# Kernel optimization log

Measured on AMD Instinct MI355X. Metric: run time of the kernel, lower is better.

## Reference

```python
import jax, jax.numpy as jnp
import numpy as np

K_MASK = -2.3819763e+38
B, T, D = 2, 2048, 2048
N, K, H = 8, 2, 256          # query heads, kv heads, head dim
F = 8192                     # ffn hidden
A = 4                        # num_altup_inputs
P = 4                        # num_modalities
WINDOW = 512
SOFT_CAP = 50.0
Q_SCALE = H ** -0.5
ROPE_BASE = 10000.0


def rms_norm(x, scale=None, eps=1e-6):
    y = x * jax.lax.rsqrt(jnp.mean(jnp.square(x), axis=-1, keepdims=True) + eps)
    if scale is not None:
        y = y * (1.0 + scale)   # scale_plus_one=True
    return y


def apply_rope(x, pos, base=ROPE_BASE, scale_factor=1.0):
    # x: [B,T,num_heads,H], pos: [B,T]
    h = x.shape[-1]
    frac = 2.0 * jnp.arange(h // 2, dtype=jnp.float32) / h
    timescale = base ** frac
    sin_inp = (pos[..., None].astype(jnp.float32) / timescale)[..., None, :] / scale_factor  # [B,T,1,H/2]
    sin, cos = jnp.sin(sin_inp), jnp.cos(sin_inp)
    x1, x2 = jnp.split(x, 2, axis=-1)
    return jnp.concatenate([x1 * cos - x2 * sin, x2 * cos + x1 * sin], axis=-1).astype(x.dtype)


def setup_inputs():
    key = jax.random.key(0)
    ks = jax.random.split(key, 12)
    r = lambda i, shape, s=0.02: jax.random.normal(ks[i], shape, dtype=jnp.float32) * s
    pos = jnp.broadcast_to(jnp.arange(T, dtype=jnp.int32), (B, T))
    causal = pos[:, :, None] >= pos[:, None, :]  # [B,T,T] bool
    return dict(
        x=jax.random.normal(ks[0], (A, B, T, D), dtype=jnp.float32),
        segment_pos=pos,
        attn_mask=causal,
        router_w=r(1, (D, P), 1.0),
        pred_coefs=r(2, (P, A, A), 0.0001),
        corr_coefs=r(3, (P, A), 0.01),
        correct_output_scale=jnp.ones((D,), jnp.float32),
        pre_attn_scale=jnp.zeros((D,), jnp.float32),
        q_w=r(4, (N, D, H)),
        kv_w=r(5, (2, K, D, H)),
        qk_q_scale=jnp.zeros((H,), jnp.float32),
        qk_k_scale=jnp.zeros((H,), jnp.float32),
        o_w=r(6, (N, H, D)),
        post_attn_scale=jnp.zeros((D,), jnp.float32),
        pre_ffw_scale=jnp.zeros((D,), jnp.float32),
        gate_w=r(7, (D, F)),
        up_w=r(8, (D, F)),
        down_w=r(9, (F, D)),
        post_ffw_scale=jnp.zeros((D,), jnp.float32),
    )


def _router(h, router_w):
    # modality router: scale by 1/d_model, project, tanh in fp32
    return jnp.tanh(jnp.einsum('btd,dp->btp', h * (1.0 / D), router_w).astype(jnp.float32))


def _attention(x, segment_pos, attn_mask, q_w, kv_w, qk_q_scale, qk_k_scale, o_w):
    q = jnp.einsum('btd,ndh->btnh', x, q_w)               # [B,T,N,H]
    k, v = jnp.einsum('bsd,ckdh->cbskh', x, kv_w)         # each [B,T,K,H]
    q = rms_norm(q, qk_q_scale)                           # qk norm
    k = rms_norm(k, qk_k_scale)
    v = rms_norm(v)                                       # value norm (no scale)
    q = apply_rope(q, segment_pos) * Q_SCALE
    k = apply_rope(k, segment_pos)
    g = N // K                                            # GQA group size
    qr = q.reshape(B, T, K, g, H)
    logits = jnp.einsum('btkgh,bskh->btkgs', qr, k).reshape(B, T, N, T)
    logits = jnp.tanh(logits / SOFT_CAP) * SOFT_CAP       # attn_logits_soft_cap
    # sliding-window mask combined with causal attn_mask
    sliding = (segment_pos[:, None, :] > segment_pos[:, :, None] - WINDOW) & \
              (segment_pos[:, None, :] < segment_pos[:, :, None] + WINDOW)
    mask = attn_mask & sliding
    padded = jnp.where(mask[:, :, None, :], logits, K_MASK)
    probs = jax.nn.softmax(padded, axis=-1).astype(k.dtype)
    enc = jnp.einsum('btkgs,bskh->btkgh', probs.reshape(B, T, K, g, T), v).reshape(B, T, N, H)
    return jnp.einsum('btnh,nhd->btd', enc, o_w)


def reference(x, segment_pos, attn_mask, router_w, pred_coefs, corr_coefs,
              correct_output_scale, pre_attn_scale, q_w, kv_w, qk_q_scale, qk_k_scale,
              o_w, post_attn_scale, pre_ffw_scale, gate_w, up_w, down_w, post_ffw_scale):
    # ---- AltUp predict ----
    mods = _router(x[0], router_w)                                   # [B,T,P]
    coefs = jnp.einsum('btp,pij->btij', mods, pred_coefs.astype(jnp.float32))
    predictions = x + jnp.einsum('btij,jbtd->ibtd', coefs, x).astype(x.dtype)
    active = predictions[0]
    # ---- attention block ----
    attn_in = rms_norm(active, pre_attn_scale)
    attn = _attention(attn_in, segment_pos, attn_mask, q_w, kv_w, qk_q_scale, qk_k_scale, o_w)
    attn = rms_norm(attn, post_attn_scale)
    attn_gated = active + attn
    # ---- gated-GELU MLP ----
    h = rms_norm(attn_gated, pre_ffw_scale)
    ffw = jnp.einsum('btf,fd->btd', jax.nn.gelu(h @ gate_w) * (h @ up_w), down_w)
    ffw = rms_norm(ffw, post_ffw_scale)
    activated = attn_gated + ffw
    # ---- AltUp correct (with scale_corrected_output) ----
    activated = activated * correct_output_scale
    mods_c = _router(activated, router_w)
    c = jnp.einsum('btp,pi->bti', mods_c, corr_coefs.astype(jnp.float32)) + 1.0
    innovation = activated - predictions[0]
    corrected = predictions + jnp.einsum('bti,btd->ibtd', c, innovation).astype(x.dtype)
    return corrected
```

## Files before the change

### kernel.cpp

```cpp
#include <hip/hip_runtime.h>
#include <hip/hip_bf16.h>

typedef unsigned short u16;
typedef __attribute__((ext_vector_type(8))) short bf16x8_t;
typedef __attribute__((ext_vector_type(4))) float f32x4_t;

#define DEV __device__ __forceinline__

constexpr int cB = 2, cT = 2048, cD = 2048;
constexpr int cN = 8, cK = 2, cH = 256, cF = 8192;
constexpr int cBT = cB * cT;
constexpr float cEPS = 1e-6f;
constexpr float cQS = 0.0625f;
constexpr float cCAP = 50.0f;
constexpr int cWIN = 512;
constexpr int cNH = 12;

DEV u16 f2bf(float f) {
  union { float f; unsigned u; } c; c.f = f;
  unsigned u = c.u;
  return (u16)((u + 0x7fffu + ((u >> 16) & 1u)) >> 16);
}
DEV float bf2f(u16 h) {
  union { unsigned u; float f; } c; c.u = ((unsigned)h) << 16;
  return c.f;
}
DEV float g4(const float4& v, int k) { return k == 0 ? v.x : k == 1 ? v.y : k == 2 ? v.z : v.w; }
DEV void store_bf4(u16* p, float a, float b, float c, float d) {
  union { u16 h[4]; uint2 v; } o;
  o.h[0] = f2bf(a); o.h[1] = f2bf(b); o.h[2] = f2bf(c); o.h[3] = f2bf(d);
  *(uint2*)p = o.v;
}
DEV float tanh_fast(float x) {
  float e2 = __expf(2.0f * x);
  return 1.0f - 2.0f * __builtin_amdgcn_rcpf(e2 + 1.0f);
}
DEV float gelu_fast(float x) {
  float u = 1.5957691216057308f * (x + 0.044715f * x * x * x);
  float e2 = __expf(u);
  return x * (1.0f - __builtin_amdgcn_rcpf(e2 + 1.0f));
}

DEV float block_sum256(float v, float* sbuf) {
  #pragma unroll
  for (int m = 32; m > 0; m >>= 1) v += __shfl_xor(v, m, 64);
  int wid = threadIdx.x >> 6;
  if ((threadIdx.x & 63) == 0) sbuf[wid] = v;
  __syncthreads();
  float tot = sbuf[0] + sbuf[1] + sbuf[2] + sbuf[3];
  __syncthreads();
  return tot;
}
DEV void block_sum256x4(float v[4], float* sbuf ) {
  #pragma unroll
  for (int m = 32; m > 0; m >>= 1) {
    #pragma unroll
    for (int k = 0; k < 4; k++) v[k] += __shfl_xor(v[k], m, 64);
  }
  int wid = threadIdx.x >> 6;
  if ((threadIdx.x & 63) == 0) *(float4*)(sbuf + wid * 4) = make_float4(v[0], v[1], v[2], v[3]);
  __syncthreads();
  #pragma unroll
  for (int k = 0; k < 4; k++) v[k] = sbuf[k] + sbuf[4 + k] + sbuf[8 + k] + sbuf[12 + k];
  __syncthreads();
}

#define GLD_LDS16(gp, lp) __builtin_amdgcn_global_load_lds( \
    (const __attribute__((address_space(1))) void*)(gp),    \
    (__attribute__((address_space(3))) void*)(lp), 16, 0, 0)

#define WAITV(n) asm volatile("s_waitcnt vmcnt(" #n ")" ::: "memory")
#define SCHED0() __builtin_amdgcn_sched_barrier(0)

__global__ __launch_bounds__(256) void k_transpose_cast(
    const float* __restrict__ src, u16* __restrict__ dst, int R, int C, int gu) {
  __shared__ float tile[64][65];
  size_t base = (size_t)blockIdx.z * R * C;
  int c0 = blockIdx.x * 64, r0 = blockIdx.y * 64;
  int tx = threadIdx.x & 15, ty = threadIdx.x >> 4;
  #pragma unroll
  for (int i = 0; i < 4; i++) {
    int r = ty + i * 16;
    float4 v = *(const float4*)(src + base + (size_t)(r0 + r) * C + c0 + tx * 4);
    tile[r][tx * 4 + 0] = v.x; tile[r][tx * 4 + 1] = v.y;
    tile[r][tx * 4 + 2] = v.z; tile[r][tx * 4 + 3] = v.w;
  }
  __syncthreads();
  #pragma unroll
  for (int i = 0; i < 4; i++) {
    int j = ty + i * 16;
    int c = c0 + j;
    int n = (gu < 0) ? c : (((c >> 4) << 5) + (gu << 4) + (c & 15));
    store_bf4(dst + base + (size_t)n * R + r0 + tx * 4,
              tile[tx * 4 + 0][j], tile[tx * 4 + 1][j],
              tile[tx * 4 + 2][j], tile[tx * 4 + 3][j]);
  }
}

__global__ __launch_bounds__(256) void k_rope_table(
    const int* __restrict__ pos, float2* __restrict__ rt) {
  int idx = blockIdx.x * 256 + threadIdx.x;
  int bt = idx >> 7, j = idx & 127;
  float p = (float)pos[bt];
  float ts = powf(10000.0f, (2.0f * j) * (1.0f / cH));
  float si = p / ts;
  rt[idx] = make_float2(sinf(si), cosf(si));
}

__global__ __launch_bounds__(256) void k_predict(
    const float* __restrict__ x, const float* __restrict__ router_w,
    const float* __restrict__ pred_coefs, const float* __restrict__ pre_attn_scale,
    float* __restrict__ out, u16* __restrict__ attn_in) {
  __shared__ float sbuf[16];
  int bt = blockIdx.x, tid = threadIdx.x;
  const size_t PL = (size_t)cBT * cD;
  const size_t rowb = (size_t)bt * cD;
  float4 xv[4][2];
  #pragma unroll
  for (int j = 0; j < 4; j++)
    #pragma unroll
    for (int u = 0; u < 2; u++)
      xv[j][u] = *(const float4*)(x + j * PL + rowb + (u * 256 + tid) * 4);
  float rp[4] = {0, 0, 0, 0};
  #pragma unroll
  for (int u = 0; u < 2; u++)
    #pragma unroll
    for (int k = 0; k < 4; k++) {
      int e = (u * 256 + tid) * 4 + k;
      float4 rw = *(const float4*)(router_w + (size_t)e * 4);
      float xe = g4(xv[0][u], k);
      rp[0] += xe * rw.x; rp[1] += xe * rw.y; rp[2] += xe * rw.z; rp[3] += xe * rw.w;
    }
  block_sum256x4(rp, sbuf);
  float mods[4];
  #pragma unroll
  for (int p = 0; p < 4; p++) mods[p] = tanh_fast(rp[p] * (1.0f / cD));
  float coef[4][4];
  #pragma unroll
  for (int i = 0; i < 4; i++)
    #pragma unroll
    for (int j = 0; j < 4; j++) {
      float s = 0;
      #pragma unroll
      for (int p = 0; p < 4; p++) s += mods[p] * pred_coefs[(p * 4 + i) * 4 + j];
      coef[i][j] = s;
    }
  float4 p04[2]; float ssq = 0;
  #pragma unroll
  for (int u = 0; u < 2; u++)
    #pragma unroll
    for (int i = 0; i < 4; i++) {
      float4 s = xv[i][u];
      #pragma unroll
      for (int j = 0; j < 4; j++) {
        s.x += coef[i][j] * xv[j][u].x; s.y += coef[i][j] * xv[j][u].y;
        s.z += coef[i][j] * xv[j][u].z; s.w += coef[i][j] * xv[j][u].w;
      }
      *(float4*)(out + i * PL + rowb + (u * 256 + tid) * 4) = s;
      if (i == 0) { p04[u] = s; ssq += s.x * s.x + s.y * s.y + s.z * s.z + s.w * s.w; }
    }
  float rs = rsqrtf(block_sum256(ssq, sbuf) * (1.0f / cD) + cEPS);
  #pragma unroll
  for (int u = 0; u < 2; u++) {
    int e0 = (u * 256 + tid) * 4;
    float4 sc = *(const float4*)(pre_attn_scale + e0);
    store_bf4(attn_in + rowb + e0,
              p04[u].x * rs * (1.0f + sc.x), p04[u].y * rs * (1.0f + sc.y),
              p04[u].z * rs * (1.0f + sc.z), p04[u].w * rs * (1.0f + sc.w));
  }
}

template <int OUT_MODE>
__global__ __launch_bounds__(512, 2) void k_gemm8w(
    const u16* __restrict__ A, const u16* __restrict__ Bt, void* __restrict__ Cv,
    int Nn, int Kk) {
  constexpr int MI = 8;
  constexpr int A_KS = 256 * 32;
  constexpr int B_KS = 256 * 32;
  constexpr int BUF_E = 2 * A_KS + 2 * B_KS;
  extern __shared__ u16 lds[];

  const int tid = threadIdx.x;
  const int wid = tid >> 6, lane = tid & 63;
  const int wr = wid >> 2, wc = wid & 3;
  const int fr = lane & 15, fq = lane >> 4;

  const int nwg = gridDim.x * gridDim.y;
  const int flat = blockIdx.y * gridDim.x + blockIdx.x;
  const int swz = (flat & 7) * (nwg >> 3) + (flat >> 3);
  const int m0 = (swz % gridDim.x) * 256;
  const int n0 = (swz / gridDim.x) * 256;
  const int NT = Kk >> 6;

  const int srow = lane >> 2, sslot = lane & 3;
  const int scol = (sslot ^ ((srow >> 1) & 3)) * 8;
  const u16* aSrc0 = A + (size_t)(m0 + wid * 16 + srow) * Kk + scol;
  const u16* aSrc1 = A + (size_t)(m0 + 128 + wid * 16 + srow) * Kk + scol;
  const u16* bSrc0 = Bt + (size_t)(n0 + wid * 16 + srow) * Kk + scol;
  const u16* bSrc1 = Bt + (size_t)(n0 + 128 + wid * 16 + srow) * Kk + scol;
  const int swzR = (fq ^ ((fr >> 1) & 3)) * 8;
  const int aoff = (wr * 128 + fr) * 32 + swzR;
  const int boff = 2 * A_KS + (wc * 64 + fr) * 32 + swzR;

  auto stageA = [&](int t, int ks) {
    u16* dst = lds + (t & 1) * BUF_E + ks * A_KS + wid * 16 * 32;
    int koff = t * 64 + ks * 32;
    GLD_LDS16(aSrc0 + koff, dst);
    GLD_LDS16(aSrc1 + koff, dst + 128 * 32);
  };
  auto stageB = [&](int t, int ks) {
    u16* dst = lds + (t & 1) * BUF_E + 2 * A_KS + ks * B_KS + wid * 16 * 32;
    int koff = t * 64 + ks * 32;
    GLD_LDS16(bSrc0 + koff, dst);
    GLD_LDS16(bSrc1 + koff, dst + 128 * 32);
  };

  f32x4_t acc[MI][4];
  #pragma unroll
  for (int i = 0; i < MI; i++)
    #pragma unroll
    for (int j = 0; j < 4; j++) acc[i][j] = (f32x4_t){0.f, 0.f, 0.f, 0.f};

  bf16x8_t a0[MI], bP[2], bQ[2];

#define RD_A(bufp, ks, i) (*(const bf16x8_t*)((bufp) + aoff + (ks) * A_KS + (i) * 512))
#define RD_B(bufp, ks, j) (*(const bf16x8_t*)((bufp) + boff + (ks) * B_KS + (j) * 512))

#define MFMA_CLUSTER(av, bv, J0)                                                     \
  __builtin_amdgcn_s_setprio(1);                                                     \
  _Pragma("unroll")                                                                  \
  for (int i = 0; i < MI; i++) {                                                     \
    acc[i][J0]     = __builtin_amdgcn_mfma_f32_16x16x32_bf16(av[i], bv[0], acc[i][J0], 0, 0, 0);     \
    acc[i][J0 + 1] = __builtin_amdgcn_mfma_f32_16x16x32_bf16(av[i], bv[1], acc[i][J0 + 1], 0, 0, 0); \
  }                                                                                  \
  __builtin_amdgcn_s_setprio(0);

  stageA(0, 0); stageB(0, 0); stageA(0, 1); stageB(0, 1);
  stageA(1, 0); stageB(1, 0);
  WAITV(8);
  __builtin_amdgcn_s_barrier();
  SCHED0();
  bP[0] = RD_B(lds, 0, 0); bP[1] = RD_B(lds, 0, 1);

  for (int t = 0; t < NT; t++) {
    const u16* buf = lds + (t & 1) * BUF_E;
    const u16* bufn = lds + ((t + 1) & 1) * BUF_E;
    const bool p1 = (t + 1 < NT), p2 = (t + 2 < NT);

    #pragma unroll
    for (int i = 0; i < MI; i++) a0[i] = RD_A(buf, 0, i);
    if (p1) stageA(t + 1, 1);
    __builtin_amdgcn_s_barrier();
    SCHED0();
    bQ[0] = RD_B(buf, 0, 2); bQ[1] = RD_B(buf, 0, 3);
    MFMA_CLUSTER(a0, bP, 0)
    __builtin_amdgcn_s_barrier();

    if (p1) stageB(t + 1, 1);
    if (p1) WAITV(8); else WAITV(0);
    __builtin_amdgcn_s_barrier();
    SCHED0();
    bP[0] = RD_B(buf, 1, 0); bP[1] = RD_B(buf, 1, 1);
    MFMA_CLUSTER(a0, bQ, 2)
    __builtin_amdgcn_s_barrier();

    #pragma unroll
    for (int i = 0; i < MI; i++) a0[i] = RD_A(buf, 1, i);
    if (p2) stageA(t + 2, 0);
    __builtin_amdgcn_s_barrier();
    SCHED0();
    bQ[0] = RD_B(buf, 1, 2); bQ[1] = RD_B(buf, 1, 3);
    MFMA_CLUSTER(a0, bP, 0)
    __builtin_amdgcn_s_barrier();

    if (p2) stageB(t + 2, 0);
    if (p2) WAITV(8); else if (p1) WAITV(4);
    __builtin_amdgcn_s_barrier();
    SCHED0();
    if (p1) { bP[0] = RD_B(bufn, 0, 0); bP[1] = RD_B(bufn, 0, 1); }
    MFMA_CLUSTER(a0, bQ, 2)
    __builtin_amdgcn_s_barrier();
  }
#undef MFMA_CLUSTER
#undef RD_A
#undef RD_B

  if constexpr (OUT_MODE == 2) {
    const int Nh = Nn >> 1;
    #pragma unroll
    for (int i = 0; i < MI; i++)
      #pragma unroll
      for (int jp = 0; jp < 2; jp++) {
        int c = (n0 + wc * 64 + jp * 32) / 2 + fr;
        #pragma unroll
        for (int r = 0; r < 4; r++) {
          int m = m0 + wr * (MI * 16) + i * 16 + fq * 4 + r;
          float g = acc[i][2 * jp][r], uu = acc[i][2 * jp + 1][r];
          ((u16*)Cv)[(size_t)m * Nh + c] = f2bf(gelu_fast(g) * uu);
        }
      }
  } else {
    #pragma unroll
    for (int i = 0; i < MI; i++)
      #pragma unroll
      for (int j = 0; j < 4; j++)
        #pragma unroll
        for (int r = 0; r < 4; r++) {
          int m = m0 + wr * (MI * 16) + i * 16 + fq * 4 + r;
          int n = n0 + wc * 64 + j * 16 + fr;
          ((u16*)Cv)[(size_t)m * Nn + n] = f2bf(acc[i][j][r]);
        }
  }
}

template <int OUT_MODE>
__global__ __launch_bounds__(512, 2) void k_gemm4r(
    const u16* __restrict__ A, const u16* __restrict__ Bt, void* __restrict__ Cv,
    int Nn, int Kk) {
  constexpr int MI = 4;
  constexpr int BM = 128;
  constexpr int A_KS = BM * 32;
  constexpr int B_KS = 256 * 32;
  constexpr int SLOT_E = 2 * A_KS + 2 * B_KS;
  extern __shared__ u16 lds[];

  const int tid = threadIdx.x;
  const int wid = tid >> 6, lane = tid & 63;
  const int wr = wid >> 2, wc = wid & 3;
  const int fr = lane & 15, fq = lane >> 4;

  const int nwg = gridDim.x * gridDim.y;
  const int flat = blockIdx.y * gridDim.x + blockIdx.x;
  const int swz = (flat & 7) * (nwg >> 3) + (flat >> 3);
  const int m0 = (swz % gridDim.x) * BM;
  const int n0 = (swz / gridDim.x) * 256;
  const int NT = Kk >> 6;

  const int srow = lane >> 2, sslot = lane & 3;

  auto stageA = [&](int t, int ks) {
    u16* buf = lds + (t % 3) * SLOT_E + ks * A_KS;
    int row0 = wid * 16;
    int row = row0 + srow;
    int col = (sslot ^ ((row >> 1) & 3)) * 8;
    GLD_LDS16(A + (size_t)(m0 + row) * Kk + t * 64 + ks * 32 + col, buf + row0 * 32);
  };
  auto stageB = [&](int t, int ks) {
    u16* buf = lds + (t % 3) * SLOT_E + 2 * A_KS + ks * B_KS;
    #pragma unroll
    for (int i = 0; i < 2; i++) {
      int row0 = i * 128 + wid * 16;
      int row = row0 + srow;
      int col = (sslot ^ ((row >> 1) & 3)) * 8;
      GLD_LDS16(Bt + (size_t)(n0 + row) * Kk + t * 64 + ks * 32 + col, buf + row0 * 32);
    }
  };
  auto readA = [&](const u16* buf, int ks, int i) -> bf16x8_t {
    int row = wr * 64 + i * 16 + fr;
    return *(const bf16x8_t*)(buf + ks * A_KS + row * 32 + (fq ^ ((row >> 1) & 3)) * 8);
  };
  auto readB = [&](const u16* buf, int ks, int j) -> bf16x8_t {
    int row = wc * 64 + j * 16 + fr;
    return *(const bf16x8_t*)(buf + 2 * A_KS + ks * B_KS + row * 32 + (fq ^ ((row >> 1) & 3)) * 8);
  };

  f32x4_t acc[MI][4];
  #pragma unroll
  for (int i = 0; i < MI; i++)
    #pragma unroll
    for (int j = 0; j < 4; j++) acc[i][j] = (f32x4_t){0.f, 0.f, 0.f, 0.f};

  stageA(0, 0); stageB(0, 0); stageA(0, 1); stageB(0, 1);
  stageA(1, 0); stageB(1, 0); stageA(1, 1); stageB(1, 1);
  WAITV(9);
  __builtin_amdgcn_s_barrier();

#define PHASE_MFMA4(J0)                                                             \
  __builtin_amdgcn_s_setprio(1);                                                    \
  _Pragma("unroll")                                                                 \
  for (int i = 0; i < MI; i++) {                                                    \
    acc[i][J0]     = __builtin_amdgcn_mfma_f32_16x16x32_bf16(a0[i], b0[0], acc[i][J0], 0, 0, 0);     \
    acc[i][J0 + 1] = __builtin_amdgcn_mfma_f32_16x16x32_bf16(a0[i], b0[1], acc[i][J0 + 1], 0, 0, 0); \
  }                                                                                 \
  __builtin_amdgcn_s_setprio(0);

  for (int t = 0; t < NT; t++) {
    const u16* buf = lds + (t % 3) * SLOT_E;
    const bool pf2 = (t + 2 < NT);
    const bool pf1 = (t + 1 < NT);
    bf16x8_t a0[MI], b0[2];

    #pragma unroll
    for (int i = 0; i < MI; i++) a0[i] = readA(buf, 0, i);
    b0[0] = readB(buf, 0, 0); b0[1] = readB(buf, 0, 1);
    if (pf2) stageA(t + 2, 0);
    __builtin_amdgcn_s_barrier();
    PHASE_MFMA4(0)
    __builtin_amdgcn_s_barrier();

    b0[0] = readB(buf, 0, 2); b0[1] = readB(buf, 0, 3);
    if (pf2) stageB(t + 2, 0);
    if (pf2) WAITV(9); else if (pf1) WAITV(6); else WAITV(0);
    __builtin_amdgcn_s_barrier();
    PHASE_MFMA4(2)
    __builtin_amdgcn_s_barrier();

    #pragma unroll
    for (int i = 0; i < MI; i++) a0[i] = readA(buf, 1, i);
    b0[0] = readB(buf, 1, 0); b0[1] = readB(buf, 1, 1);
    if (pf2) stageA(t + 2, 1);
    __builtin_amdgcn_s_barrier();
    PHASE_MFMA4(0)
    __builtin_amdgcn_s_barrier();

    b0[0] = readB(buf, 1, 2); b0[1] = readB(buf, 1, 3);
    if (pf2) stageB(t + 2, 1);
    if (pf2) WAITV(9); else if (pf1) WAITV(3);
    __builtin_amdgcn_s_barrier();
    PHASE_MFMA4(2)
    __builtin_amdgcn_s_barrier();
  }
#undef PHASE_MFMA4

  #pragma unroll
  for (int i = 0; i < MI; i++)
    #pragma unroll
    for (int j = 0; j < 4; j++)
      #pragma unroll
      for (int r = 0; r < 4; r++) {
        int m = m0 + wr * 64 + i * 16 + fq * 4 + r;
        int n = n0 + wc * 64 + j * 16 + fr;
        float v = acc[i][j][r];
        if (OUT_MODE == 1) ((u16*)Cv)[(size_t)m * Nn + n] = f2bf(v);
        else ((float*)Cv)[(size_t)m * Nn + n] = v;
      }
}

__global__ __launch_bounds__(64) void k_qkvpost(
    u16* __restrict__ qkv, const float* __restrict__ qscale,
    const float* __restrict__ kscale, const float2* __restrict__ rt,
    u16* __restrict__ vT) {
  int h = blockIdx.x % cNH, bt = blockIdx.x / cNH;
  int lane = threadIdx.x;
  u16* row = qkv + ((size_t)bt * cNH + h) * cH;
  float v[4], ssq = 0;
  #pragma unroll
  for (int m = 0; m < 4; m++) { v[m] = bf2f(row[lane + 64 * m]); ssq += v[m] * v[m]; }
  #pragma unroll
  for (int mm = 32; mm > 0; mm >>= 1) ssq += __shfl_xor(ssq, mm, 64);
  float rs = rsqrtf(ssq * (1.0f / cH) + cEPS);
  if (h < 10) {
    const float* sc = (h < 8) ? qscale : kscale;
    float os = (h < 8) ? cQS : 1.0f;
    #pragma unroll
    for (int m = 0; m < 4; m++) {
      int e = lane + 64 * m;
      v[m] = v[m] * rs * (1.0f + sc[e]);
    }
    #pragma unroll
    for (int m = 0; m < 2; m++) {
      int j = lane + 64 * m;
      float2 t = rt[bt * 128 + j];
      float x1 = v[m], x2 = v[m + 2];
      row[j]       = f2bf((x1 * t.y - x2 * t.x) * os);
      row[j + 128] = f2bf((x2 * t.y + x1 * t.x) * os);
    }
  } else {
    int kk = h - 10;
    int b = bt / cT, t = bt % cT;
    #pragma unroll
    for (int m = 0; m < 4; m++) {
      int e = lane + 64 * m;
      vT[((size_t)(b * cK + kk) * cH + e) * cT + t] = f2bf(v[m] * rs);
    }
  }
}

__global__ __launch_bounds__(64) void k_attn(
    const u16* __restrict__ qkv, const u16* __restrict__ vT, u16* __restrict__ enc) {
  int t0 = blockIdx.x * 16;
  int n = blockIdx.y, b = blockIdx.z;
  int kn = n >> 2;
  int lane = threadIdx.x;
  int fr = lane & 15, fq = lane >> 4;
  __shared__ float P[16][33];

  bf16x8_t qf[8];
  const u16* qrow = qkv + ((size_t)(b * cT + t0 + fr) * cNH + n) * cH;
  #pragma unroll
  for (int ks = 0; ks < 8; ks++) qf[ks] = *(const bf16x8_t*)(qrow + ks * 32 + fq * 8);

  f32x4_t acc[16];
  #pragma unroll
  for (int ht = 0; ht < 16; ht++) acc[ht] = (f32x4_t){0.f, 0.f, 0.f, 0.f};
  float psum[4] = {0.f, 0.f, 0.f, 0.f};

  int s_lo = t0 - (cWIN - 1); if (s_lo < 0) s_lo = 0; s_lo &= ~31;
  for (int s0 = s_lo; s0 <= t0 + 15; s0 += 32) {
    f32x4_t S[2];
    S[0] = (f32x4_t){0.f, 0.f, 0.f, 0.f};
    S[1] = (f32x4_t){0.f, 0.f, 0.f, 0.f};
    #pragma unroll
    for (int c = 0; c < 2; c++) {
      const u16* krow = qkv + ((size_t)(b * cT + s0 + c * 16 + fr) * cNH + 8 + kn) * cH;
      #pragma unroll
      for (int ks = 0; ks < 8; ks++) {
        bf16x8_t kf = *(const bf16x8_t*)(krow + ks * 32 + fq * 8);
        S[c] = __builtin_amdgcn_mfma_f32_16x16x32_bf16(qf[ks], kf, S[c], 0, 0, 0);
      }
    }
    #pragma unroll
    for (int c = 0; c < 2; c++) {
      int s = s0 + c * 16 + fr;
      #pragma unroll
      for (int r = 0; r < 4; r++) {
        int t = t0 + fq * 4 + r;
        float l = cCAP * tanh_fast(S[c][r] * (1.0f / cCAP));
        float pe = (s <= t && s >= t - (cWIN - 1)) ? __expf(l) : 0.0f;
        psum[r] += pe;
        P[fq * 4 + r][c * 16 + fr] = pe;
      }
    }
    bf16x8_t pf;
    #pragma unroll
    for (int e = 0; e < 8; e++) pf[e] = (short)f2bf(P[fr][fq * 8 + e]);
    #pragma unroll
    for (int ht = 0; ht < 16; ht++) {
      bf16x8_t vf = *(const bf16x8_t*)(vT + (((size_t)(b * cK + kn)) * cH + ht * 16 + fr) * cT + s0 + fq * 8);
      acc[ht] = __builtin_amdgcn_mfma_f32_16x16x32_bf16(pf, vf, acc[ht], 0, 0, 0);
    }
  }
  #pragma unroll
  for (int r = 0; r < 4; r++) {
    #pragma unroll
    for (int m = 1; m < 16; m <<= 1) psum[r] += __shfl_xor(psum[r], m, 64);
  }
  float inv[4];
  #pragma unroll
  for (int r = 0; r < 4; r++) inv[r] = 1.0f / psum[r];
  #pragma unroll
  for (int ht = 0; ht < 16; ht++)
    #pragma unroll
    for (int r = 0; r < 4; r++)
      enc[(((size_t)(b * cT + t0 + fq * 4 + r)) * cN + n) * cH + ht * 16 + fr] =
          f2bf(acc[ht][r] * inv[r]);
}

__global__ __launch_bounds__(256) void k_postattn(
    const float* __restrict__ attn_raw, const float* __restrict__ out0,
    const float* __restrict__ post_attn_scale, const float* __restrict__ pre_ffw_scale,
    float* __restrict__ ag, u16* __restrict__ h) {
  __shared__ float sbuf[4];
  int bt = blockIdx.x, tid = threadIdx.x;
  const size_t rowb = (size_t)bt * cD;
  float4 ar[2]; float ssq = 0;
  #pragma unroll
  for (int u = 0; u < 2; u++) {
    ar[u] = *(const float4*)(attn_raw + rowb + (u * 256 + tid) * 4);
    ssq += ar[u].x * ar[u].x + ar[u].y * ar[u].y + ar[u].z * ar[u].z + ar[u].w * ar[u].w;
  }
  float rs = rsqrtf(block_sum256(ssq, sbuf) * (1.0f / cD) + cEPS);
  float4 agv[2]; float ssq2 = 0;
  #pragma unroll
  for (int u = 0; u < 2; u++) {
    int e0 = (u * 256 + tid) * 4;
    float4 o0 = *(const float4*)(out0 + rowb + e0);
    float4 sc = *(const float4*)(post_attn_scale + e0);
    float4 a;
    a.x = o0.x + ar[u].x * rs * (1.0f + sc.x);
    a.y = o0.y + ar[u].y * rs * (1.0f + sc.y);
    a.z = o0.z + ar[u].z * rs * (1.0f + sc.z);
    a.w = o0.w + ar[u].w * rs * (1.0f + sc.w);
    agv[u] = a;
    *(float4*)(ag + rowb + e0) = a;
    ssq2 += a.x * a.x + a.y * a.y + a.z * a.z + a.w * a.w;
  }
  float rs2 = rsqrtf(block_sum256(ssq2, sbuf) * (1.0f / cD) + cEPS);
  #pragma unroll
  for (int u = 0; u < 2; u++) {
    int e0 = (u * 256 + tid) * 4;
    float4 sc = *(const float4*)(pre_ffw_scale + e0);
    store_bf4(h + rowb + e0,
              agv[u].x * rs2 * (1.0f + sc.x), agv[u].y * rs2 * (1.0f + sc.y),
              agv[u].z * rs2 * (1.0f + sc.z), agv[u].w * rs2 * (1.0f + sc.w));
  }
}

__global__ __launch_bounds__(256) void k_final(
    const float* __restrict__ ffw_raw, const float* __restrict__ ag,
    const float* __restrict__ post_ffw_scale, const float* __restrict__ cos_scale,
    const float* __restrict__ router_w, const float* __restrict__ corr_coefs,
    float* __restrict__ out) {
  __shared__ float sbuf[16];
  int bt = blockIdx.x, tid = threadIdx.x;
  const size_t PL = (size_t)cBT * cD;
  const size_t rowb = (size_t)bt * cD;
  float4 fv[2]; float ssq = 0;
  #pragma unroll
  for (int u = 0; u < 2; u++) {
    fv[u] = *(const float4*)(ffw_raw + rowb + (u * 256 + tid) * 4);
    ssq += fv[u].x * fv[u].x + fv[u].y * fv[u].y + fv[u].z * fv[u].z + fv[u].w * fv[u].w;
  }
  float rs = rsqrtf(block_sum256(ssq, sbuf) * (1.0f / cD) + cEPS);
  float4 av[2];
  float rp[4] = {0, 0, 0, 0};
  #pragma unroll
  for (int u = 0; u < 2; u++) {
    int e0 = (u * 256 + tid) * 4;
    float4 agx = *(const float4*)(ag + rowb + e0);
    float4 ps = *(const float4*)(post_ffw_scale + e0);
    float4 cs = *(const float4*)(cos_scale + e0);
    float4 a;
    a.x = (agx.x + fv[u].x * rs * (1.0f + ps.x)) * cs.x;
    a.y = (agx.y + fv[u].y * rs * (1.0f + ps.y)) * cs.y;
    a.z = (agx.z + fv[u].z * rs * (1.0f + ps.z)) * cs.z;
    a.w = (agx.w + fv[u].w * rs * (1.0f + ps.w)) * cs.w;
    av[u] = a;
    #pragma unroll
    for (int k = 0; k < 4; k++) {
      float4 rw = *(const float4*)(router_w + (size_t)(e0 + k) * 4);
      float xe = g4(a, k);
      rp[0] += xe * rw.x; rp[1] += xe * rw.y; rp[2] += xe * rw.z; rp[3] += xe * rw.w;
    }
  }
  block_sum256x4(rp, sbuf);
  float cc[4];
  #pragma unroll
  for (int i = 0; i < 4; i++) {
    float s = 1.0f;
    #pragma unroll
    for (int p = 0; p < 4; p++) s += tanh_fast(rp[p] * (1.0f / cD)) * corr_coefs[p * 4 + i];
    cc[i] = s;
  }
  #pragma unroll
  for (int u = 0; u < 2; u++) {
    size_t o = rowb + (u * 256 + tid) * 4;
    float4 p0 = *(const float4*)(out + o);
    float4 in4;
    in4.x = av[u].x - p0.x; in4.y = av[u].y - p0.y;
    in4.z = av[u].z - p0.z; in4.w = av[u].w - p0.w;
    float4 w0;
    w0.x = p0.x + cc[0] * in4.x; w0.y = p0.y + cc[0] * in4.y;
    w0.z = p0.z + cc[0] * in4.z; w0.w = p0.w + cc[0] * in4.w;
    *(float4*)(out + o) = w0;
    #pragma unroll
    for (int i = 1; i < 4; i++) {
      float4 q = *(const float4*)(out + i * PL + o);
      q.x += cc[i] * in4.x; q.y += cc[i] * in4.y;
      q.z += cc[i] * in4.z; q.w += cc[i] * in4.w;
      *(float4*)(out + i * PL + o) = q;
    }
  }
}

extern "C" void kernel_launch(void* const* d_in, const int* in_sizes, int n_in,
                              void* d_out, int out_size, void* d_ws, size_t ws_size,
                              hipStream_t stream) {
  const float* x              = (const float*)d_in[0];
  const int*   pos            = (const int*)d_in[1];
  const float* router_w       = (const float*)d_in[3];
  const float* pred_coefs     = (const float*)d_in[4];
  const float* corr_coefs     = (const float*)d_in[5];
  const float* cos_scale      = (const float*)d_in[6];
  const float* pre_attn_scale = (const float*)d_in[7];
  const float* q_w            = (const float*)d_in[8];
  const float* kv_w           = (const float*)d_in[9];
  const float* qk_q_scale     = (const float*)d_in[10];
  const float* qk_k_scale     = (const float*)d_in[11];
  const float* o_w            = (const float*)d_in[12];
  const float* post_attn_scale= (const float*)d_in[13];
  const float* pre_ffw_scale  = (const float*)d_in[14];
  const float* gate_w         = (const float*)d_in[15];
  const float* up_w           = (const float*)d_in[16];
  const float* down_w         = (const float*)d_in[17];
  const float* post_ffw_scale = (const float*)d_in[18];
  float* out = (float*)d_out;

  char* wsp = (char*)d_ws;
  size_t off = 0;
  auto take = [&](size_t nbytes) -> char* {
    char* p = wsp + off;
    off += (nbytes + 255) & ~((size_t)255);
    return p;
  };
  u16* gu_wT    = (u16*)take((size_t)2 * cF * cD * 2);
  u16* down_wT  = (u16*)take((size_t)cD * cF * 2);
  u16* qkv_wT   = (u16*)take((size_t)cNH * cH * cD * 2);
  u16* o_wT     = (u16*)take((size_t)cD * cN * cH * 2);
  u16* attn_in  = (u16*)take((size_t)cBT * cD * 2);
  u16* qkvbuf   = (u16*)take((size_t)cBT * cNH * cH * 2);
  u16* vTbuf    = (u16*)take((size_t)cB * cK * cH * cT * 2);
  u16* encbuf   = (u16*)take((size_t)cBT * cN * cH * 2);
  float* attn_raw = (float*)take((size_t)cBT * cD * 4);
  float* agbuf    = (float*)take((size_t)cBT * cD * 4);
  u16* hbuf     = (u16*)take((size_t)cBT * cD * 2);
  u16* Gcbuf    = (u16*)take((size_t)cBT * cF * 2);
  float* ffw_raw = (float*)take((size_t)cBT * cD * 4);
  float2* ropetab = (float2*)take((size_t)cBT * 128 * 8);
  (void)in_sizes; (void)n_in; (void)out_size; (void)ws_size;

  dim3 blk256(256), blk64(64), blk512(512);
  constexpr unsigned LDS8  = 2 * (2 * 256 * 32 + 2 * 256 * 32) * 2;
  constexpr unsigned LDS4R = 3 * (2 * 128 * 32 + 2 * 256 * 32) * 2;

  k_transpose_cast<<<dim3(cF / 64, cD / 64, 1), blk256, 0, stream>>>(gate_w, gu_wT, cD, cF, 0);
  k_transpose_cast<<<dim3(cF / 64, cD / 64, 1), blk256, 0, stream>>>(up_w, gu_wT, cD, cF, 1);
  k_transpose_cast<<<dim3(cD / 64, cF / 64, 1), blk256, 0, stream>>>(down_w, down_wT, cF, cD, -1);
  k_transpose_cast<<<dim3(cH / 64, cD / 64, cN), blk256, 0, stream>>>(q_w, qkv_wT, cD, cH, -1);
  k_transpose_cast<<<dim3(cH / 64, cD / 64, 2 * cK), blk256, 0, stream>>>(
      kv_w, qkv_wT + (size_t)cN * cH * cD, cD, cH, -1);
  k_transpose_cast<<<dim3(cD / 64, (cN * cH) / 64, 1), blk256, 0, stream>>>(o_w, o_wT, cN * cH, cD, -1);
  k_rope_table<<<dim3(cBT * 128 / 256), blk256, 0, stream>>>(pos, ropetab);

  k_predict<<<dim3(cBT), blk256, 0, stream>>>(x, router_w, pred_coefs, pre_attn_scale, out, attn_in);

  k_gemm4r<1><<<dim3(cBT / 128, (cNH * cH) / 256), blk512, LDS4R, stream>>>(
      attn_in, qkv_wT, qkvbuf, cNH * cH, cD);

  k_qkvpost<<<dim3(cBT * cNH), blk64, 0, stream>>>(qkvbuf, qk_q_scale, qk_k_scale, ropetab, vTbuf);

  k_attn<<<dim3(cT / 16, cN, cB), blk64, 0, stream>>>(qkvbuf, vTbuf, encbuf);

  k_gemm4r<0><<<dim3(cBT / 128, cD / 256), blk512, LDS4R, stream>>>(
      encbuf, o_wT, attn_raw, cD, cN * cH);
  k_postattn<<<dim3(cBT), blk256, 0, stream>>>(attn_raw, out, post_attn_scale, pre_ffw_scale, agbuf, hbuf);

  k_gemm8w<2><<<dim3(cBT / 256, (2 * cF) / 256), blk512, LDS8, stream>>>(
      hbuf, gu_wT, Gcbuf, 2 * cF, cD);
  k_gemm4r<0><<<dim3(cBT / 128, cD / 256), blk512, LDS4R, stream>>>(
      Gcbuf, down_wT, ffw_raw, cD, cF);

  k_final<<<dim3(cBT), blk256, 0, stream>>>(ffw_raw, agbuf, post_ffw_scale, cos_scale,
                                            router_w, corr_coefs, out);
}
```

Measured before the change: 952.2 us.

## Restructure gate/up GEMM main loop into half-tile register double-buffered pipeline

Measured after the change: 950.5 us. Within noise of the previous version (-0.2%).

```diff
diff --git a/kernel.cpp b/kernel.cpp
--- a/kernel.cpp
+++ b/kernel.cpp
@@ -70,7 +70,11 @@
     (__attribute__((address_space(3))) void*)(lp), 16, 0, 0)
 
 #define WAITV(n) asm volatile("s_waitcnt vmcnt(" #n ")" ::: "memory")
+#define LGKM(n)  asm volatile("s_waitcnt lgkmcnt(" #n ")" ::: "memory")
 #define SCHED0() __builtin_amdgcn_sched_barrier(0)
+#define LDS_ADDR(p) ((unsigned)(uintptr_t)(__attribute__((address_space(3))) const void*)(p))
+#define DSR(dst, base, off) \
+  asm volatile("ds_read_b128 %0, %1 offset:" off : "=v"(dst) : "v"(base))
 
 __global__ __launch_bounds__(256) void k_transpose_cast(
     const float* __restrict__ src, u16* __restrict__ dst, int R, int C, int gu) {
@@ -171,7 +175,7 @@
 }
 
 template <int OUT_MODE>
-__global__ __launch_bounds__(512, 2) void k_gemm8w(
+__global__ __launch_bounds__(512, 2) void k_gemm8p(
     const u16* __restrict__ A, const u16* __restrict__ Bt, void* __restrict__ Cv,
     int Nn, int Kk) {
   constexpr int MI = 8;
@@ -191,6 +195,7 @@
   const int m0 = (swz % gridDim.x) * 256;
   const int n0 = (swz / gridDim.x) * 256;
   const int NT = Kk >> 6;
+  const int NH = NT * 2;
 
   const int srow = lane >> 2, sslot = lane & 3;
   const int scol = (sslot ^ ((srow >> 1) & 3)) * 8;
@@ -198,22 +203,24 @@
   const u16* aSrc1 = A + (size_t)(m0 + 128 + wid * 16 + srow) * Kk + scol;
   const u16* bSrc0 = Bt + (size_t)(n0 + wid * 16 + srow) * Kk + scol;
   const u16* bSrc1 = Bt + (size_t)(n0 + 128 + wid * 16 + srow) * Kk + scol;
+
   const int swzR = (fq ^ ((fr >> 1) & 3)) * 8;
-  const int aoff = (wr * 128 + fr) * 32 + swzR;
-  const int boff = 2 * A_KS + (wc * 64 + fr) * 32 + swzR;
-
-  auto stageA = [&](int t, int ks) {
-    u16* dst = lds + (t & 1) * BUF_E + ks * A_KS + wid * 16 * 32;
-    int koff = t * 64 + ks * 32;
-    GLD_LDS16(aSrc0 + koff, dst);
-    GLD_LDS16(aSrc1 + koff, dst + 128 * 32);
+  const unsigned base0 = LDS_ADDR(lds);
+  const unsigned aoffB = (unsigned)(((wr * 128 + fr) * 32 + swzR) * 2);
+  const unsigned boffB = (unsigned)((2 * A_KS + (wc * 64 + fr) * 32 + swzR) * 2);
+  const unsigned aB0 = base0 + aoffB, aB1 = base0 + BUF_E * 2 + aoffB;
+  const unsigned bB0 = base0 + boffB, bB1 = base0 + BUF_E * 2 + boffB;
+
+  auto stageH = [&](int h) {
+    int tt = h >> 1, ks = h & 1;
+    int koff = h * 32;
+    u16* dstA = lds + (tt & 1) * BUF_E + ks * A_KS + wid * 512;
+    GLD_LDS16(aSrc0 + koff, dstA);
+    GLD_LDS16(aSrc1 + koff, dstA + 128 * 32);
+    u16* dstB = lds + (tt & 1) * BUF_E + 2 * A_KS + ks * B_KS + wid * 512;
+    GLD_LDS16(bSrc0 + koff, dstB);
+    GLD_LDS16(bSrc1 + koff, dstB + 128 * 32);
   };
-  auto stageB = [&](int t, int ks) {
-    u16* dst = lds + (t & 1) * BUF_E + 2 * A_KS + ks * B_KS + wid * 16 * 32;
-    int koff = t * 64 + ks * 32;
-    GLD_LDS16(bSrc0 + koff, dst);
-    GLD_LDS16(bSrc1 + koff, dst + 128 * 32);
-  };
 
   f32x4_t acc[MI][4];
   #pragma unroll
@@ -221,69 +228,78 @@
     #pragma unroll
     for (int j = 0; j < 4; j++) acc[i][j] = (f32x4_t){0.f, 0.f, 0.f, 0.f};
 
-  bf16x8_t a0[MI], bP[2], bQ[2];
-
-#define RD_A(bufp, ks, i) (*(const bf16x8_t*)((bufp) + aoff + (ks) * A_KS + (i) * 512))
-#define RD_B(bufp, ks, j) (*(const bf16x8_t*)((bufp) + boff + (ks) * B_KS + (j) * 512))
-
-#define MFMA_CLUSTER(av, bv, J0)                                                     \
-  __builtin_amdgcn_s_setprio(1);                                                     \
-  _Pragma("unroll")                                                                  \
-  for (int i = 0; i < MI; i++) {                                                     \
-    acc[i][J0]     = __builtin_amdgcn_mfma_f32_16x16x32_bf16(av[i], bv[0], acc[i][J0], 0, 0, 0);     \
-    acc[i][J0 + 1] = __builtin_amdgcn_mfma_f32_16x16x32_bf16(av[i], bv[1], acc[i][J0 + 1], 0, 0, 0); \
-  }                                                                                  \
+  bf16x8_t aX[8], aY[8], bX[4], bY[4];
+
+#define READS_KS0(ab, bb, av, bv) do {                                   \
+    DSR(av[0], ab, "0");     DSR(av[1], ab, "1024");                     \
+    DSR(av[2], ab, "2048");  DSR(av[3], ab, "3072");                     \
+    DSR(av[4], ab, "4096");  DSR(av[5], ab, "5120");                     \
+    DSR(av[6], ab, "6144");  DSR(av[7], ab, "7168");                     \
+    DSR(bv[0], bb, "0");     DSR(bv[1], bb, "1024");                     \
+    DSR(bv[2], bb, "2048");  DSR(bv[3], bb, "3072");  } while (0)
+#define READS_KS1(ab, bb, av, bv) do {                                   \
+    DSR(av[0], ab, "16384"); DSR(av[1], ab, "17408");                    \
+    DSR(av[2], ab, "18432"); DSR(av[3], ab, "19456");                    \
+    DSR(av[4], ab, "20480"); DSR(av[5], ab, "21504");                    \
+    DSR(av[6], ab, "22528"); DSR(av[7], ab, "23552");                    \
+    DSR(bv[0], bb, "16384"); DSR(bv[1], bb, "17408");                    \
+    DSR(bv[2], bb, "18432"); DSR(bv[3], bb, "19456"); } while (0)
+
+#define MFMA32(av, bv)                                                    \
+  __builtin_amdgcn_s_setprio(1);                                          \
+  _Pragma("unroll")                                                       \
+  for (int i = 0; i < 8; i++) {                                           \
+    acc[i][0] = __builtin_amdgcn_mfma_f32_16x16x32_bf16(av[i], bv[0], acc[i][0], 0, 0, 0); \
+    acc[i][1] = __builtin_amdgcn_mfma_f32_16x16x32_bf16(av[i], bv[1], acc[i][1], 0, 0, 0); \
+    acc[i][2] = __builtin_amdgcn_mfma_f32_16x16x32_bf16(av[i], bv[2], acc[i][2], 0, 0, 0); \
+    acc[i][3] = __builtin_amdgcn_mfma_f32_16x16x32_bf16(av[i], bv[3], acc[i][3], 0, 0, 0); \
+  }                                                                       \
   __builtin_amdgcn_s_setprio(0);
 
-  stageA(0, 0); stageB(0, 0); stageA(0, 1); stageB(0, 1);
-  stageA(1, 0); stageB(1, 0);
+  stageH(0); asm volatile("" ::: "memory");
+  stageH(1); asm volatile("" ::: "memory");
+  stageH(2);
   WAITV(8);
   __builtin_amdgcn_s_barrier();
   SCHED0();
-  bP[0] = RD_B(lds, 0, 0); bP[1] = RD_B(lds, 0, 1);
+  READS_KS0(aB0, bB0, aX, bX);
 
   for (int t = 0; t < NT; t++) {
-    const u16* buf = lds + (t & 1) * BUF_E;
-    const u16* bufn = lds + ((t + 1) & 1) * BUF_E;
-    const bool p1 = (t + 1 < NT), p2 = (t + 2 < NT);
-
-    #pragma unroll
-    for (int i = 0; i < MI; i++) a0[i] = RD_A(buf, 0, i);
-    if (p1) stageA(t + 1, 1);
-    __builtin_amdgcn_s_barrier();
-    SCHED0();
-    bQ[0] = RD_B(buf, 0, 2); bQ[1] = RD_B(buf, 0, 3);
-    MFMA_CLUSTER(a0, bP, 0)
-    __builtin_amdgcn_s_barrier();
-
-    if (p1) stageB(t + 1, 1);
-    if (p1) WAITV(8); else WAITV(0);
-    __builtin_amdgcn_s_barrier();
-    SCHED0();
-    bP[0] = RD_B(buf, 1, 0); bP[1] = RD_B(buf, 1, 1);
-    MFMA_CLUSTER(a0, bQ, 2)
-    __builtin_amdgcn_s_barrier();
-
-    #pragma unroll
-    for (int i = 0; i < MI; i++) a0[i] = RD_A(buf, 1, i);
-    if (p2) stageA(t + 2, 0);
-    __builtin_amdgcn_s_barrier();
-    SCHED0();
-    bQ[0] = RD_B(buf, 1, 2); bQ[1] = RD_B(buf, 1, 3);
-    MFMA_CLUSTER(a0, bP, 0)
-    __builtin_amdgcn_s_barrier();
-
-    if (p2) stageB(t + 2, 0);
-    if (p2) WAITV(8); else if (p1) WAITV(4);
-    __builtin_amdgcn_s_barrier();
-    SCHED0();
-    if (p1) { bP[0] = RD_B(bufn, 0, 0); bP[1] = RD_B(bufn, 0, 1); }
-    MFMA_CLUSTER(a0, bQ, 2)
-    __builtin_amdgcn_s_barrier();
-  }
-#undef MFMA_CLUSTER
-#undef RD_A
-#undef RD_B
+    const unsigned aPb = (t & 1) ? aB1 : aB0;
+    const unsigned bPb = (t & 1) ? bB1 : bB0;
+    const unsigned aNb = (t & 1) ? aB0 : aB1;
+    const unsigned bNb = (t & 1) ? bB0 : bB1;
+
+    {
+      const int R = NH - 1 - 2 * t;
+      if (R >= 2) WAITV(4); else WAITV(0);
+      __builtin_amdgcn_s_barrier();
+      SCHED0();
+      if (R >= 3) stageH(2 * t + 3);
+      READS_KS1(aPb, bPb, aY, bY);
+      LGKM(12);
+      SCHED0();
+      MFMA32(aX, bX)
+    }
+    {
+      const int R = NH - 2 - 2 * t;
+      if (R >= 2) WAITV(4); else if (R == 1) WAITV(0);
+      __builtin_amdgcn_s_barrier();
+      SCHED0();
+      if (R >= 3) stageH(2 * t + 4);
+      if (R >= 1) {
+        READS_KS0(aNb, bNb, aX, bX);
+        LGKM(12);
+      } else {
+        LGKM(0);
+      }
+      SCHED0();
+      MFMA32(aY, bY)
+    }
+  }
+#undef MFMA32
+#undef READS_KS0
+#undef READS_KS1
 
   if constexpr (OUT_MODE == 2) {
     const int Nh = Nn >> 1;
@@ -725,7 +741,7 @@
       encbuf, o_wT, attn_raw, cD, cN * cH);
   k_postattn<<<dim3(cBT), blk256, 0, stream>>>(attn_raw, out, post_attn_scale, pre_ffw_scale, agbuf, hbuf);
 
-  k_gemm8w<2><<<dim3(cBT / 256, (2 * cF) / 256), blk512, LDS8, stream>>>(
+  k_gemm8p<2><<<dim3(cBT / 256, (2 * cF) / 256), blk512, LDS8, stream>>>(
       hbuf, gu_wT, Gcbuf, 2 * cF, cD);
   k_gemm4r<0><<<dim3(cBT / 128, cD / 256), blk512, LDS4R, stream>>>(
       Gcbuf, down_wT, ffw_raw, cD, cF);
```
